# Kernel optimization log

Hardware: AMD Instinct MI355X
Metric: run time of the kernel (lower is better)

## Reference

```python
import jax, jax.numpy as jnp
import numpy as np

SEQ_LEN = 1024
CHANNELS = 64
UNITS = 32
WIDTH = 64
BATCH = 4
EPS = 1e-7


def setup_inputs() -> dict:
    key = jax.random.key(0)
    ks = jax.random.split(key, 5)
    x = jax.random.normal(ks[0], (BATCH, CHANNELS, SEQ_LEN), dtype=jnp.float32)
    Wt = jax.random.normal(ks[1], (UNITS, CHANNELS), dtype=jnp.float32) * (1.0 / np.sqrt(CHANNELS))
    Wx = jax.random.normal(ks[2], (UNITS, CHANNELS), dtype=jnp.float32) * (1.0 / np.sqrt(CHANNELS))
    Wa_w = jax.random.normal(ks[3], (1, UNITS), dtype=jnp.float32) * (1.0 / np.sqrt(UNITS))
    Wa_b = jnp.zeros((1,), dtype=jnp.float32)
    bh = jnp.zeros((UNITS,), dtype=jnp.float32)
    return {"x": x, "Wt": Wt, "Wx": Wx, "Wa_w": Wa_w, "Wa_b": Wa_b, "bh": bh}


def reference(x, Wt, Wx, Wa_w, Wa_b, bh):
    # x: (B, C, S) -> xt: (B, S, C)
    xt = jnp.transpose(x, (0, 2, 1))
    q = jnp.einsum('bsc,uc->bsu', xt, Wt)          # (B, S, U)
    k = jnp.einsum('bsc,uc->bsu', xt, Wx)          # (B, S, U)
    # additive (Bahdanau) scores: tanh over broadcast sum -> (B, S, S, U)
    h = jnp.tanh(q[:, :, None, :] + k[:, None, :, :] + bh)
    e = jnp.einsum('bstu,u->bst', h, Wa_w[0]) + Wa_b[0]   # (B, S, S)
    e = jnp.exp(e - jnp.max(e, axis=-1, keepdims=True))
    # local window mask: key index t allowed for query s iff s-W//2 <= t < s-W//2+W
    idx = jnp.arange(SEQ_LEN)
    lower = idx - WIDTH // 2                        # (S,)
    mask = (lower[:, None] <= idx[None, :]) & (idx[None, :] < (lower[:, None] + WIDTH))
    e = e * mask.astype(e.dtype)
    a = e / (jnp.sum(e, axis=-1, keepdims=True) + EPS)    # (B, S, S)
    v = jnp.einsum('bst,btc->bsc', a, xt)           # (B, S, C)
    v = jnp.transpose(v, (0, 2, 1))                 # (B, C, S)
    return (v, a)
```

## Files before the change

### kernel.cpp

```cpp
#include <hip/hip_runtime.h>
#include <cstddef>
#include <cmath>

#define SEQ    1024
#define CH     64
#define UNITS  32
#define WIDTH  64
#define HALFW  32
#define BATCH  4
#define EPS    1e-7f

#define TS     8
#define TT     72
#define XS     73
#define SCS    65

__global__ __launch_bounds__(256) void qk_kernel(
    const float* __restrict__ x, const float* __restrict__ Wt,
    const float* __restrict__ Wx, float* __restrict__ q, float* __restrict__ k)
{
    int bu = blockIdx.x;
    int u  = bu & (UNITS - 1);
    int b  = bu >> 5;
    int s4 = (int)threadIdx.x << 2;

    const float* wt = Wt + u * CH;
    const float* wx = Wx + u * CH;
    const float* xb = x + (size_t)b * CH * SEQ + s4;

    float4 qa = {0.f, 0.f, 0.f, 0.f};
    float4 ka = {0.f, 0.f, 0.f, 0.f};
#pragma unroll
    for (int c = 0; c < CH; ++c) {
        float4 xv = *reinterpret_cast<const float4*>(xb + (size_t)c * SEQ);
        float wtc = wt[c], wxc = wx[c];
        qa.x = fmaf(xv.x, wtc, qa.x); qa.y = fmaf(xv.y, wtc, qa.y);
        qa.z = fmaf(xv.z, wtc, qa.z); qa.w = fmaf(xv.w, wtc, qa.w);
        ka.x = fmaf(xv.x, wxc, ka.x); ka.y = fmaf(xv.y, wxc, ka.y);
        ka.z = fmaf(xv.z, wxc, ka.z); ka.w = fmaf(xv.w, wxc, ka.w);
    }
    size_t o = (size_t)bu * SEQ + s4;
    *reinterpret_cast<float4*>(q + o) = qa;
    *reinterpret_cast<float4*>(k + o) = ka;
}

__global__ __launch_bounds__(256) void attn_kernel(
    const float* __restrict__ x,
    const float* __restrict__ q, const float* __restrict__ k,
    const float* __restrict__ Wa_w, const float* __restrict__ Wa_b,
    const float* __restrict__ bh, float* __restrict__ out)
{
    __shared__ float xt[CH * XS];
    __shared__ float kt[UNITS * XS];
    __shared__ float qt[UNITS * TS];
    __shared__ float sc[TS * SCS];
    __shared__ float wa_s[UNITS], bh_s[UNITS];
    __shared__ float wab_s;

    int tid = threadIdx.x;
    int blk = blockIdx.x;
    int b   = blk >> 7;
    int s0  = (blk & 127) << 3;
    int t0  = s0 - HALFW;

    const float* xb = x + (size_t)b * CH * SEQ;
    const float* qb = q + (size_t)b * UNITS * SEQ;
    const float* kb = k + (size_t)b * UNITS * SEQ;

    {
        int u = tid >> 3, sl = tid & 7;
        qt[u * TS + sl] = qb[u * SEQ + s0 + sl];
    }
    if (tid < UNITS) { wa_s[tid] = Wa_w[tid]; bh_s[tid] = bh[tid]; }
    if (tid == 0)    { wab_s = Wa_b[0]; }
#pragma unroll
    for (int i = 0; i < 9; ++i) {
        int idx = i * 256 + tid;
        int u = idx / TT, tt = idx - u * TT;
        int t = t0 + tt; t = t < 0 ? 0 : (t >= SEQ ? SEQ - 1 : t);
        kt[u * XS + tt] = kb[u * SEQ + t];
    }
#pragma unroll
    for (int i = 0; i < 18; ++i) {
        int idx = i * 256 + tid;
        int c = idx / TT, tt = idx - c * TT;
        int t = t0 + tt; t = t < 0 ? 0 : (t >= SEQ ? SEQ - 1 : t);
        xt[c * XS + tt] = xb[c * SEQ + t];
    }
    __syncthreads();

    {
        int sl = tid >> 5, tlg = tid & 31;
        float e0 = wab_s, e1 = wab_s;
#pragma unroll
        for (int u = 0; u < UNITS; ++u) {
            float qv = qt[u * TS + sl] + bh_s[u];
            float k0 = kt[u * XS + sl + tlg];
            float k1 = kt[u * XS + sl + tlg + 32];
            float wa = wa_s[u];
            float z0 = qv + k0, z1 = qv + k1;
            float th0 = 1.f - 2.f * __builtin_amdgcn_rcpf(__expf(2.f * z0) + 1.f);
            float th1 = 1.f - 2.f * __builtin_amdgcn_rcpf(__expf(2.f * z1) + 1.f);
            e0 = fmaf(th0, wa, e0);
            e1 = fmaf(th1, wa, e1);
        }
        int ta = t0 + sl + tlg, tb = t0 + sl + tlg + 32;
        if (ta < 0 || ta >= SEQ) e0 = -INFINITY;
        if (tb < 0 || tb >= SEQ) e1 = -INFINITY;
        sc[sl * SCS + tlg]      = e0;
        sc[sl * SCS + tlg + 32] = e1;
    }
    __syncthreads();

    {
        int lane = tid & 63, wv = tid >> 6;
        int row  = wv * 2 + (lane >> 5);
        int l32  = lane & 31;
        float e0 = sc[row * SCS + l32];
        float e1 = sc[row * SCS + l32 + 32];
        float m = fmaxf(e0, e1);
#pragma unroll
        for (int off = 16; off >= 1; off >>= 1) m = fmaxf(m, __shfl_xor(m, off));
        float p0 = __expf(e0 - m), p1 = __expf(e1 - m);
        float ssum = p0 + p1;
#pragma unroll
        for (int off = 16; off >= 1; off >>= 1) ssum += __shfl_xor(ssum, off);
        float inv = __builtin_amdgcn_rcpf(ssum + EPS);
        sc[row * SCS + l32]      = p0 * inv;
        sc[row * SCS + l32 + 32] = p1 * inv;
    }
    __syncthreads();

    float* arow = out + (size_t)BATCH * CH * SEQ + ((size_t)(b * SEQ + s0)) * SEQ;
    int i0 = tid << 2;
#pragma unroll
    for (int r = 0; r < TS; ++r) {
        int lowerAbs = s0 + r - HALFW;
        int d = i0 - lowerAbs;
        float4 v4 = {0.f, 0.f, 0.f, 0.f};
        if (d > -4 && d < WIDTH) {
            const float* row = sc + r * SCS;
            if (d >= 0     && d     < WIDTH) v4.x = row[d];
            if (d + 1 >= 0 && d + 1 < WIDTH) v4.y = row[d + 1];
            if (d + 2 >= 0 && d + 2 < WIDTH) v4.z = row[d + 2];
            if (d + 3 >= 0 && d + 3 < WIDTH) v4.w = row[d + 3];
        }
        *reinterpret_cast<float4*>(arow + (size_t)r * SEQ + i0) = v4;
    }

    {
        int slv = tid & 7, c0 = (tid >> 3) << 1;
        float acc0 = 0.f, acc1 = 0.f;
        const float* x0 = xt + c0 * XS + slv;
        const float* x1 = x0 + XS;
        const float* ar = sc + slv * SCS;
#pragma unroll
        for (int j = 0; j < WIDTH; ++j) {
            float av = ar[j];
            acc0 = fmaf(av, x0[j], acc0);
            acc1 = fmaf(av, x1[j], acc1);
        }
        out[((size_t)(b * CH + c0)) * SEQ + s0 + slv]     = acc0;
        out[((size_t)(b * CH + c0 + 1)) * SEQ + s0 + slv] = acc1;
    }
}

extern "C" void kernel_launch(void* const* d_in, const int* in_sizes, int n_in,
                              void* d_out, int out_size, void* d_ws, size_t ws_size,
                              hipStream_t stream) {
    const float* x    = (const float*)d_in[0];
    const float* Wt   = (const float*)d_in[1];
    const float* Wx   = (const float*)d_in[2];
    const float* Wa_w = (const float*)d_in[3];
    const float* Wa_b = (const float*)d_in[4];
    const float* bh   = (const float*)d_in[5];
    float* out = (float*)d_out;

    float* q  = (float*)d_ws;
    float* kk = q + (size_t)BATCH * UNITS * SEQ;

    qk_kernel<<<BATCH * UNITS, 256, 0, stream>>>(x, Wt, Wx, q, kk);
    attn_kernel<<<BATCH * (SEQ / TS), 256, 0, stream>>>(x, q, kk, Wa_w, Wa_b, bh, out);
}
```

Measured before the change: 81.02 us.

## Split attention into score and value kernels, fold tanh constants, vectorize loads

The fused attention kernel is split into a score kernel, which writes the attention matrix, and a value kernel, which reads the attention rows back from output memory and computes v. The q/k projection now folds in the bias and the factor of two, and the tanh is rewritten as a sigmoid-style reciprocal with the weights prescaled by -2, dropping Wa_b since the softmax shift cancels it. Interior tiles load their windows with float4 and a padded stride of 76. q and k are parked in the v region of the output, which v_kernel later overwrites. The cost is a third launch and an extra read of the attention window from global memory.

Result: slower. 83.68 us (+3.3%).

```diff
diff --git a/kernel.cpp b/kernel.cpp
--- a/kernel.cpp
+++ b/kernel.cpp
@@ -12,12 +12,14 @@
 
 #define TS     8
 #define TT     72
-#define XS     73
+#define XS     76
 #define SCS    65
+
 
 __global__ __launch_bounds__(256) void qk_kernel(
     const float* __restrict__ x, const float* __restrict__ Wt,
-    const float* __restrict__ Wx, float* __restrict__ q, float* __restrict__ k)
+    const float* __restrict__ Wx, const float* __restrict__ bh,
+    float* __restrict__ q2, float* __restrict__ k2)
 {
     int bu = blockIdx.x;
     int u  = bu & (UNITS - 1);
@@ -39,23 +41,24 @@
         ka.x = fmaf(xv.x, wxc, ka.x); ka.y = fmaf(xv.y, wxc, ka.y);
         ka.z = fmaf(xv.z, wxc, ka.z); ka.w = fmaf(xv.w, wxc, ka.w);
     }
+    float bhu = bh[u];
+    qa.x = 2.f * (qa.x + bhu); qa.y = 2.f * (qa.y + bhu);
+    qa.z = 2.f * (qa.z + bhu); qa.w = 2.f * (qa.w + bhu);
+    ka.x *= 2.f; ka.y *= 2.f; ka.z *= 2.f; ka.w *= 2.f;
+
     size_t o = (size_t)bu * SEQ + s4;
-    *reinterpret_cast<float4*>(q + o) = qa;
-    *reinterpret_cast<float4*>(k + o) = ka;
-}
-
-__global__ __launch_bounds__(256) void attn_kernel(
-    const float* __restrict__ x,
-    const float* __restrict__ q, const float* __restrict__ k,
-    const float* __restrict__ Wa_w, const float* __restrict__ Wa_b,
-    const float* __restrict__ bh, float* __restrict__ out)
+    *reinterpret_cast<float4*>(q2 + o) = qa;
+    *reinterpret_cast<float4*>(k2 + o) = ka;
+}
+
+__global__ __launch_bounds__(256) void score_kernel(
+    const float* __restrict__ q2, const float* __restrict__ k2,
+    const float* __restrict__ Wa_w, float* __restrict__ aout)
 {
-    __shared__ float xt[CH * XS];
     __shared__ float kt[UNITS * XS];
     __shared__ float qt[UNITS * TS];
     __shared__ float sc[TS * SCS];
-    __shared__ float wa_s[UNITS], bh_s[UNITS];
-    __shared__ float wab_s;
+    __shared__ float wa_s[UNITS];
 
     int tid = threadIdx.x;
     int blk = blockIdx.x;
@@ -63,46 +66,49 @@
     int s0  = (blk & 127) << 3;
     int t0  = s0 - HALFW;
 
-    const float* xb = x + (size_t)b * CH * SEQ;
-    const float* qb = q + (size_t)b * UNITS * SEQ;
-    const float* kb = k + (size_t)b * UNITS * SEQ;
+    const float* qb = q2 + (size_t)b * UNITS * SEQ;
+    const float* kb = k2 + (size_t)b * UNITS * SEQ;
 
     {
         int u = tid >> 3, sl = tid & 7;
         qt[u * TS + sl] = qb[u * SEQ + s0 + sl];
     }
-    if (tid < UNITS) { wa_s[tid] = Wa_w[tid]; bh_s[tid] = bh[tid]; }
-    if (tid == 0)    { wab_s = Wa_b[0]; }
-#pragma unroll
-    for (int i = 0; i < 9; ++i) {
-        int idx = i * 256 + tid;
-        int u = idx / TT, tt = idx - u * TT;
-        int t = t0 + tt; t = t < 0 ? 0 : (t >= SEQ ? SEQ - 1 : t);
-        kt[u * XS + tt] = kb[u * SEQ + t];
-    }
-#pragma unroll
-    for (int i = 0; i < 18; ++i) {
-        int idx = i * 256 + tid;
-        int c = idx / TT, tt = idx - c * TT;
-        int t = t0 + tt; t = t < 0 ? 0 : (t >= SEQ ? SEQ - 1 : t);
-        xt[c * XS + tt] = xb[c * SEQ + t];
+    if (tid < UNITS) wa_s[tid] = -2.f * Wa_w[tid];
+
+    if (t0 >= 0 && t0 + TT <= SEQ) {
+#pragma unroll
+        for (int i = 0; i < 3; ++i) {
+            int idx = i * 256 + tid;
+            if (idx < UNITS * 18) {
+                int u = idx / 18, p = idx - u * 18;
+                float4 v4 = *reinterpret_cast<const float4*>(kb + u * SEQ + t0 + (p << 2));
+                *reinterpret_cast<float4*>(&kt[u * XS + (p << 2)]) = v4;
+            }
+        }
+    } else {
+#pragma unroll
+        for (int i = 0; i < 9; ++i) {
+            int idx = i * 256 + tid;
+            int u = idx / TT, tt = idx - u * TT;
+            int t = t0 + tt; t = t < 0 ? 0 : (t >= SEQ ? SEQ - 1 : t);
+            kt[u * XS + tt] = kb[u * SEQ + t];
+        }
     }
     __syncthreads();
 
     {
         int sl = tid >> 5, tlg = tid & 31;
-        float e0 = wab_s, e1 = wab_s;
+        float e0 = 0.f, e1 = 0.f;
 #pragma unroll
         for (int u = 0; u < UNITS; ++u) {
-            float qv = qt[u * TS + sl] + bh_s[u];
+            float qv = qt[u * TS + sl];
             float k0 = kt[u * XS + sl + tlg];
             float k1 = kt[u * XS + sl + tlg + 32];
             float wa = wa_s[u];
-            float z0 = qv + k0, z1 = qv + k1;
-            float th0 = 1.f - 2.f * __builtin_amdgcn_rcpf(__expf(2.f * z0) + 1.f);
-            float th1 = 1.f - 2.f * __builtin_amdgcn_rcpf(__expf(2.f * z1) + 1.f);
-            e0 = fmaf(th0, wa, e0);
-            e1 = fmaf(th1, wa, e1);
+            float r0 = __builtin_amdgcn_rcpf(__expf(qv + k0) + 1.f);
+            float r1 = __builtin_amdgcn_rcpf(__expf(qv + k1) + 1.f);
+            e0 = fmaf(wa, r0, e0);
+            e1 = fmaf(wa, r1, e1);
         }
         int ta = t0 + sl + tlg, tb = t0 + sl + tlg + 32;
         if (ta < 0 || ta >= SEQ) e0 = -INFINITY;
@@ -131,7 +137,7 @@
     }
     __syncthreads();
 
-    float* arow = out + (size_t)BATCH * CH * SEQ + ((size_t)(b * SEQ + s0)) * SEQ;
+    float* arow = aout + ((size_t)(b * SEQ + s0)) * SEQ;
     int i0 = tid << 2;
 #pragma unroll
     for (int r = 0; r < TS; ++r) {
@@ -147,6 +153,55 @@
         }
         *reinterpret_cast<float4*>(arow + (size_t)r * SEQ + i0) = v4;
     }
+}
+
+__global__ __launch_bounds__(256) void v_kernel(
+    const float* __restrict__ x, const float* __restrict__ aout,
+    float* __restrict__ out)
+{
+    __shared__ float xt[CH * XS];
+    __shared__ float sc[TS * SCS];
+
+    int tid = threadIdx.x;
+    int blk = blockIdx.x;
+    int b   = blk >> 7;
+    int s0  = (blk & 127) << 3;
+    int t0  = s0 - HALFW;
+
+    const float* xb = x + (size_t)b * CH * SEQ;
+
+    if (t0 >= 0 && t0 + TT <= SEQ) {
+#pragma unroll
+        for (int i = 0; i < 5; ++i) {
+            int idx = i * 256 + tid;
+            if (idx < CH * 18) {
+                int c = idx / 18, p = idx - c * 18;
+                float4 v4 = *reinterpret_cast<const float4*>(xb + c * SEQ + t0 + (p << 2));
+                *reinterpret_cast<float4*>(&xt[c * XS + (p << 2)]) = v4;
+            }
+        }
+    } else {
+#pragma unroll
+        for (int i = 0; i < 18; ++i) {
+            int idx = i * 256 + tid;
+            int c = idx / TT, tt = idx - c * TT;
+            int t = t0 + tt; t = t < 0 ? 0 : (t >= SEQ ? SEQ - 1 : t);
+            xt[c * XS + tt] = xb[c * SEQ + t];
+        }
+    }
+
+    {
+        const float* ab = aout + ((size_t)(b * SEQ + s0)) * SEQ;
+#pragma unroll
+        for (int i = 0; i < 2; ++i) {
+            int idx = i * 256 + tid;
+            int r = idx >> 6, j = idx & 63;
+            int t = t0 + r + j;
+            float av = (t >= 0 && t < SEQ) ? ab[(size_t)r * SEQ + t] : 0.f;
+            sc[r * SCS + j] = av;
+        }
+    }
+    __syncthreads();
 
     {
         int slv = tid & 7, c0 = (tid >> 3) << 1;
@@ -172,13 +227,14 @@
     const float* Wt   = (const float*)d_in[1];
     const float* Wx   = (const float*)d_in[2];
     const float* Wa_w = (const float*)d_in[3];
-    const float* Wa_b = (const float*)d_in[4];
     const float* bh   = (const float*)d_in[5];
     float* out = (float*)d_out;
 
-    float* q  = (float*)d_ws;
-    float* kk = q + (size_t)BATCH * UNITS * SEQ;
-
-    qk_kernel<<<BATCH * UNITS, 256, 0, stream>>>(x, Wt, Wx, q, kk);
-    attn_kernel<<<BATCH * (SEQ / TS), 256, 0, stream>>>(x, q, kk, Wa_w, Wa_b, bh, out);
-}
+    float* q2   = out;
+    float* k2   = out + (size_t)BATCH * UNITS * SEQ;
+    float* aout = out + (size_t)BATCH * CH * SEQ;
+
+    qk_kernel<<<BATCH * UNITS, 256, 0, stream>>>(x, Wt, Wx, bh, q2, k2);
+    score_kernel<<<BATCH * (SEQ / TS), 256, 0, stream>>>(q2, k2, Wa_w, aout);
+    v_kernel<<<BATCH * (SEQ / TS), 256, 0, stream>>>(x, aout, out);
+}
```
